# Kernel optimization log

Measured on AMD Instinct MI355X. Metric: run time of the kernel, lower is better.

## Reference

```python
import jax, jax.numpy as jnp
import numpy as np

EPS = 1e-5

def setup_inputs() -> dict:
    key = jax.random.key(0)
    ks = jax.random.split(key, 6)
    D, V, N = 2048, 30000, 4096
    return {
        "x": jax.random.normal(ks[0], (N, D), dtype=jnp.float32),
        "w1": jax.random.normal(ks[1], (D, D), dtype=jnp.float32) * (1.0 / np.sqrt(D)),
        "b1": jax.random.normal(ks[2], (D,), dtype=jnp.float32) * 0.02,
        "gamma": jnp.ones((D,), dtype=jnp.float32),
        "beta": jnp.zeros((D,), dtype=jnp.float32),
        "w3": jax.random.normal(ks[3], (V, D), dtype=jnp.float32) * (1.0 / np.sqrt(D)),
        "b3": jax.random.normal(ks[4], (V,), dtype=jnp.float32) * 0.02,
    }

def reference(x, w1, b1, gamma, beta, w3, b3):
    # Stage 1: Linear 2048 -> 2048 (torch convention: y = x @ W.T + b)
    h = jnp.einsum('nd,od->no', x, w1) + b1  # [N, 2048]
    # Stage 2: fused LayerNorm + Linear 2048 -> 30000
    mu = jnp.mean(h, axis=-1, keepdims=True)
    var = jnp.mean(jnp.square(h - mu), axis=-1, keepdims=True)
    hn = (h - mu) * jax.lax.rsqrt(var + EPS) * gamma + beta
    logits = jnp.einsum('nd,vd->nv', hn, w3) + b3  # [N, 30000]
    return logits
```

## Files before the change

### kernel.cpp

```cpp
#include <hip/hip_runtime.h>
#include <hip/hip_bf16.h>
#include <stdint.h>

typedef __attribute__((ext_vector_type(8))) short bf16x8;
typedef __attribute__((ext_vector_type(4))) float f32x4;

__device__ __forceinline__ uint16_t f2bf(float f) {
  uint32_t u = __builtin_bit_cast(uint32_t, f);
  u += 0x7fffu + ((u >> 16) & 1u);
  return (uint16_t)(u >> 16);
}

__global__ __launch_bounds__(256) void cvt_bf16(const float* __restrict__ in,
                                                uint16_t* __restrict__ out,
                                                size_t n8) {
  size_t i = (size_t)blockIdx.x * blockDim.x + threadIdx.x;
  size_t stride = (size_t)gridDim.x * blockDim.x;
  for (; i < n8; i += stride) {
    const float4* p = reinterpret_cast<const float4*>(in) + 2 * i;
    float4 a = p[0], b = p[1];
    uint4 o;
    o.x = (uint32_t)f2bf(a.x) | ((uint32_t)f2bf(a.y) << 16);
    o.y = (uint32_t)f2bf(a.z) | ((uint32_t)f2bf(a.w) << 16);
    o.z = (uint32_t)f2bf(b.x) | ((uint32_t)f2bf(b.y) << 16);
    o.w = (uint32_t)f2bf(b.z) | ((uint32_t)f2bf(b.w) << 16);
    reinterpret_cast<uint4*>(out)[i] = o;
  }
}

__global__ __launch_bounds__(256) void cvt_bf16_pad(const float* __restrict__ in,
                                                    uint16_t* __restrict__ out,
                                                    int rows_in, size_t n8) {
  size_t i = (size_t)blockIdx.x * blockDim.x + threadIdx.x;
  size_t stride = (size_t)gridDim.x * blockDim.x;
  for (; i < n8; i += stride) {
    size_t row = (i * 8) >> 11;
    uint4 o;
    if (row < (size_t)rows_in) {
      const float4* p = reinterpret_cast<const float4*>(in) + 2 * i;
      float4 a = p[0], b = p[1];
      o.x = (uint32_t)f2bf(a.x) | ((uint32_t)f2bf(a.y) << 16);
      o.y = (uint32_t)f2bf(a.z) | ((uint32_t)f2bf(a.w) << 16);
      o.z = (uint32_t)f2bf(b.x) | ((uint32_t)f2bf(b.y) << 16);
      o.w = (uint32_t)f2bf(b.z) | ((uint32_t)f2bf(b.w) << 16);
    } else {
      o.x = 0u; o.y = 0u; o.z = 0u; o.w = 0u;
    }
    reinterpret_cast<uint4*>(out)[i] = o;
  }
}

#define GLOAD16(g, l) __builtin_amdgcn_global_load_lds(                         \
    (__attribute__((address_space(1))) const void*)(g),                         \
    (__attribute__((address_space(3))) void*)(l), 16, 0, 0)

__global__ __launch_bounds__(256, 2) void gemm_bt_bf16(
    const uint16_t* __restrict__ A, const uint16_t* __restrict__ B,
    float* __restrict__ C, const float* __restrict__ bias,
    int M, int Npad, int K, int Nout)
{
  constexpr int BM = 128, BN = 128, BK = 32;
  __shared__ uint16_t sA[BM * BK];
  __shared__ uint16_t sB[BN * BK];

  const int ntile = Npad / BN;
  const int mtile = M / BM;
  const int nwg = ntile * mtile;
  const int bid = blockIdx.x;
  const int cpx = nwg >> 3;
  const int swz = (bid & 7) * cpx + (bid >> 3);
  const int tm = swz % mtile;
  const int tn = swz / mtile;

  const int tid = threadIdx.x;
  const int lane = tid & 63;
  const int wid = tid >> 6;
  const int wm = wid >> 1;
  const int wn = wid & 1;

  const int srow = tid >> 2;
  const int scol = (tid & 3) * 8;
  const uint16_t* ga0 = A + (size_t)(tm * BM + srow) * K + scol;
  const uint16_t* ga1 = ga0 + (size_t)64 * K;
  const uint16_t* gb0 = B + (size_t)(tn * BN + srow) * K + scol;
  const uint16_t* gb1 = gb0 + (size_t)64 * K;
  uint16_t* lA = sA + wid * 512;
  uint16_t* lB = sB + wid * 512;

  const int arow = wm * 64 + (lane & 15);
  const int brow = wn * 64 + (lane & 15);
  const int koff = (lane >> 4) * 8;

  f32x4 acc[4][4];
  #pragma unroll
  for (int m = 0; m < 4; ++m)
    #pragma unroll
    for (int n = 0; n < 4; ++n)
      acc[m][n] = (f32x4){0.f, 0.f, 0.f, 0.f};

  for (int k0 = 0; k0 < K; k0 += BK) {
    __syncthreads();
    GLOAD16(ga0, lA);
    GLOAD16(ga1, lA + 2048);
    GLOAD16(gb0, lB);
    GLOAD16(gb1, lB + 2048);
    ga0 += BK; ga1 += BK; gb0 += BK; gb1 += BK;
    __syncthreads();

    bf16x8 af[4], bfr[4];
    #pragma unroll
    for (int m = 0; m < 4; ++m)
      af[m] = *reinterpret_cast<const bf16x8*>(&sA[(arow + m * 16) * BK + koff]);
    #pragma unroll
    for (int n = 0; n < 4; ++n)
      bfr[n] = *reinterpret_cast<const bf16x8*>(&sB[(brow + n * 16) * BK + koff]);
    #pragma unroll
    for (int m = 0; m < 4; ++m)
      #pragma unroll
      for (int n = 0; n < 4; ++n)
        acc[m][n] = __builtin_amdgcn_mfma_f32_16x16x32_bf16(af[m], bfr[n],
                                                            acc[m][n], 0, 0, 0);
  }

  const int r0 = tm * BM + wm * 64 + (lane >> 4) * 4;
  const int c0 = tn * BN + wn * 64 + (lane & 15);
  #pragma unroll
  for (int m = 0; m < 4; ++m) {
    #pragma unroll
    for (int n = 0; n < 4; ++n) {
      const int c = c0 + n * 16;
      if (c < Nout) {
        const float bv = bias ? bias[c] : 0.f;
        #pragma unroll
        for (int j = 0; j < 4; ++j)
          C[(size_t)(r0 + m * 16 + j) * Nout + c] = acc[m][n][j] + bv;
      }
    }
  }
}

__global__ __launch_bounds__(256) void ln_bf16(
    const float* __restrict__ h, const float* __restrict__ b1,
    const float* __restrict__ gamma, const float* __restrict__ beta,
    uint16_t* __restrict__ out)
{
  constexpr int D = 2048;
  const int row = blockIdx.x;
  const int tid = threadIdx.x;
  const float* hp = h + (size_t)row * D + tid * 8;
  float v[8];
  {
    float4 a0 = *reinterpret_cast<const float4*>(hp);
    float4 a1 = *reinterpret_cast<const float4*>(hp + 4);
    float4 c0 = *reinterpret_cast<const float4*>(b1 + tid * 8);
    float4 c1 = *reinterpret_cast<const float4*>(b1 + tid * 8 + 4);
    v[0] = a0.x + c0.x; v[1] = a0.y + c0.y; v[2] = a0.z + c0.z; v[3] = a0.w + c0.w;
    v[4] = a1.x + c1.x; v[5] = a1.y + c1.y; v[6] = a1.z + c1.z; v[7] = a1.w + c1.w;
  }
  float s = 0.f, q = 0.f;
  #pragma unroll
  for (int i = 0; i < 8; ++i) { s += v[i]; q += v[i] * v[i]; }
  #pragma unroll
  for (int off = 32; off > 0; off >>= 1) {
    s += __shfl_down(s, off);
    q += __shfl_down(q, off);
  }
  __shared__ float red[8];
  const int wid = tid >> 6, lane = tid & 63;
  if (lane == 0) { red[wid] = s; red[4 + wid] = q; }
  __syncthreads();
  s = red[0] + red[1] + red[2] + red[3];
  q = red[4] + red[5] + red[6] + red[7];
  const float mu = s * (1.f / D);
  const float rs = rsqrtf(q * (1.f / D) - mu * mu + 1e-5f);
  float4 g0 = *reinterpret_cast<const float4*>(gamma + tid * 8);
  float4 g1 = *reinterpret_cast<const float4*>(gamma + tid * 8 + 4);
  float4 e0 = *reinterpret_cast<const float4*>(beta + tid * 8);
  float4 e1 = *reinterpret_cast<const float4*>(beta + tid * 8 + 4);
  const float g[8] = {g0.x, g0.y, g0.z, g0.w, g1.x, g1.y, g1.z, g1.w};
  const float e[8] = {e0.x, e0.y, e0.z, e0.w, e1.x, e1.y, e1.z, e1.w};
  uint32_t w[4];
  #pragma unroll
  for (int i = 0; i < 4; ++i) {
    float y0 = (v[2 * i]     - mu) * rs * g[2 * i]     + e[2 * i];
    float y1 = (v[2 * i + 1] - mu) * rs * g[2 * i + 1] + e[2 * i + 1];
    w[i] = (uint32_t)f2bf(y0) | ((uint32_t)f2bf(y1) << 16);
  }
  uint4 o; o.x = w[0]; o.y = w[1]; o.z = w[2]; o.w = w[3];
  reinterpret_cast<uint4*>(out + (size_t)row * D)[tid] = o;
}

extern "C" void kernel_launch(void* const* d_in, const int* in_sizes, int n_in,
                              void* d_out, int out_size, void* d_ws, size_t ws_size,
                              hipStream_t stream) {
  (void)in_sizes; (void)n_in; (void)out_size; (void)ws_size;
  const float* x     = (const float*)d_in[0];
  const float* w1    = (const float*)d_in[1];
  const float* b1    = (const float*)d_in[2];
  const float* gamma = (const float*)d_in[3];
  const float* beta  = (const float*)d_in[4];
  const float* w3    = (const float*)d_in[5];
  const float* b3    = (const float*)d_in[6];
  float* out = (float*)d_out;

  const int N = 4096, D = 2048, V = 30000, Vp = 30080;

  char* ws = (char*)d_ws;
  uint16_t* xb  = (uint16_t*)(ws);
  uint16_t* w1b = (uint16_t*)(ws + (16u  << 20));
  float*    h   = (float*)   (ws + (24u  << 20));
  uint16_t* hnb = (uint16_t*)(ws + (56u  << 20));
  uint16_t* w3b = (uint16_t*)(ws + (72u  << 20));

  hipLaunchKernelGGL(cvt_bf16, dim3(1024), dim3(256), 0, stream,
                     x, xb, (size_t)N * D / 8);
  hipLaunchKernelGGL(cvt_bf16, dim3(512), dim3(256), 0, stream,
                     w1, w1b, (size_t)D * D / 8);
  hipLaunchKernelGGL(cvt_bf16_pad, dim3(2048), dim3(256), 0, stream,
                     w3, w3b, V, (size_t)Vp * D / 8);
  hipLaunchKernelGGL(gemm_bt_bf16, dim3((N / 128) * (D / 128)), dim3(256), 0, stream,
                     xb, w1b, h, (const float*)nullptr, N, D, D, D);
  hipLaunchKernelGGL(ln_bf16, dim3(N), dim3(256), 0, stream,
                     h, b1, gamma, beta, hnb);
  hipLaunchKernelGGL(gemm_bt_bf16, dim3((N / 128) * (Vp / 128)), dim3(256), 0, stream,
                     hnb, w3b, out, b3, N, Vp, D, V);
}
```

Before: 1.371 ms.

## Add 256x256-tile multi-stage pipelined GEMM for vocab projection

Adds a 512-thread GEMM kernel with 256x256 output tiles and a four-buffer LDS ring (128KB) that keeps three global-to-LDS stages in flight, synchronised with explicit vmcnt waits and barriers. The large logits projection now uses this kernel, with the vocabulary padding raised to a multiple of 256. The goal is more operand reuse per LDS load and memory latency hidden behind MFMA work. The workspace is reshuffled and the w3 conversion moved after the layernorm so the bf16 weight buffer can reuse space no longer needed. The cost is higher register and LDS pressure, which limits the kernel to one workgroup per CU, plus slightly more wasted padding work.

```diff
diff --git a/kernel.cpp b/kernel.cpp
--- a/kernel.cpp
+++ b/kernel.cpp
@@ -139,6 +139,99 @@
   }
 }
 
+__global__ __launch_bounds__(512, 2) void gemm_bt_256(
+    const uint16_t* __restrict__ A, const uint16_t* __restrict__ B,
+    float* __restrict__ C, const float* __restrict__ bias,
+    int M, int Npad, int K, int Nout)
+{
+  __shared__ char lds[131072];
+  constexpr int BM = 256, BN = 256, BK = 32;
+  const int ntile = Npad / BN;
+  const int mtile = M / BM;
+  const int nwg = ntile * mtile;
+  const int bid = blockIdx.x;
+  const int cpx = nwg >> 3;
+  const int swz = (bid & 7) * cpx + (bid >> 3);
+  const int tm = swz % mtile;
+  const int tn = swz / mtile;
+
+  const int tid = threadIdx.x;
+  const int lane = tid & 63;
+  const int wid = tid >> 6;
+  const int wm = wid >> 2;
+  const int wn = wid & 3;
+
+  const size_t K_ = (size_t)K;
+  const uint16_t* gA = A + (size_t)(tm * BM + (tid >> 2)) * K_ + (tid & 3) * 8;
+  const uint16_t* gB = B + (size_t)(tn * BN + (tid >> 2)) * K_ + (tid & 3) * 8;
+  const size_t halfs = 128 * K_;
+  const int stageBase = wid * 1024;
+
+  const int nt = K / BK;
+
+  const int rd   = (lane & 15) * 64 + (lane >> 4) * 16;
+  const int aoff = wm * 8192 + rd;
+  const int boff = wn * 4096 + rd;
+
+  f32x4 acc[8][4];
+  #pragma unroll
+  for (int r = 0; r < 8; ++r)
+    #pragma unroll
+    for (int n = 0; n < 4; ++n)
+      acc[r][n] = (f32x4){0.f, 0.f, 0.f, 0.f};
+
+#define STAGE256(b, koff)                                                     \
+  { char* d = lds + (b) * 32768 + stageBase;                                  \
+    GLOAD16(gA + (koff),          d);                                         \
+    GLOAD16(gA + halfs + (koff),  d + 8192);                                  \
+    GLOAD16(gB + (koff),          d + 16384);                                 \
+    GLOAD16(gB + halfs + (koff),  d + 24576); }
+
+  STAGE256(0, 0); STAGE256(1, 32); STAGE256(2, 64);
+
+  for (int t = 0; t < nt; ++t) {
+    const int rem = nt - 1 - t;
+    if (rem >= 2)      asm volatile("s_waitcnt vmcnt(8)" ::: "memory");
+    else if (rem == 1) asm volatile("s_waitcnt vmcnt(4)" ::: "memory");
+    else               asm volatile("s_waitcnt vmcnt(0)" ::: "memory");
+    asm volatile("s_barrier" ::: "memory");
+    if (t + 3 < nt) STAGE256((t + 3) & 3, (t + 3) * BK);
+
+    const char* bA = lds + (t & 3) * 32768;
+    const char* bB = bA + 16384;
+    bf16x8 bF[4], aF[8];
+    #pragma unroll
+    for (int n = 0; n < 4; ++n)
+      bF[n] = *reinterpret_cast<const bf16x8*>(bB + boff + n * 1024);
+    #pragma unroll
+    for (int r = 0; r < 8; ++r)
+      aF[r] = *reinterpret_cast<const bf16x8*>(bA + aoff + r * 1024);
+    #pragma unroll
+    for (int r = 0; r < 8; ++r)
+      #pragma unroll
+      for (int n = 0; n < 4; ++n)
+        acc[r][n] = __builtin_amdgcn_mfma_f32_16x16x32_bf16(aF[r], bF[n],
+                                                            acc[r][n], 0, 0, 0);
+  }
+#undef STAGE256
+
+  const int r0 = tm * BM + wm * 128 + (lane >> 4) * 4;
+  const int c0 = tn * BN + wn * 64 + (lane & 15);
+  #pragma unroll
+  for (int r = 0; r < 8; ++r) {
+    #pragma unroll
+    for (int n = 0; n < 4; ++n) {
+      const int c = c0 + n * 16;
+      if (c < Nout) {
+        const float bv = bias ? bias[c] : 0.f;
+        #pragma unroll
+        for (int j = 0; j < 4; ++j)
+          C[(size_t)(r0 + r * 16 + j) * Nout + c] = acc[r][n][j] + bv;
+      }
+    }
+  }
+}
+
 __global__ __launch_bounds__(256) void ln_bf16(
     const float* __restrict__ h, const float* __restrict__ b1,
     const float* __restrict__ gamma, const float* __restrict__ beta,
@@ -203,25 +296,25 @@
   const float* b3    = (const float*)d_in[6];
   float* out = (float*)d_out;
 
-  const int N = 4096, D = 2048, V = 30000, Vp = 30080;
+  const int N = 4096, D = 2048, V = 30000, Vp = 30208;
 
   char* ws = (char*)d_ws;
-  uint16_t* xb  = (uint16_t*)(ws);
-  uint16_t* w1b = (uint16_t*)(ws + (16u  << 20));
-  float*    h   = (float*)   (ws + (24u  << 20));
-  uint16_t* hnb = (uint16_t*)(ws + (56u  << 20));
-  uint16_t* w3b = (uint16_t*)(ws + (72u  << 20));
+  uint16_t* hnb = (uint16_t*)(ws);
+  float*    h   = (float*)   (ws + (16u << 20));
+  uint16_t* xb  = (uint16_t*)(ws + (48u << 20));
+  uint16_t* w1b = (uint16_t*)(ws + (64u << 20));
+  uint16_t* w3b = (uint16_t*)(ws + (24u << 20));
 
   hipLaunchKernelGGL(cvt_bf16, dim3(1024), dim3(256), 0, stream,
                      x, xb, (size_t)N * D / 8);
   hipLaunchKernelGGL(cvt_bf16, dim3(512), dim3(256), 0, stream,
                      w1, w1b, (size_t)D * D / 8);
-  hipLaunchKernelGGL(cvt_bf16_pad, dim3(2048), dim3(256), 0, stream,
-                     w3, w3b, V, (size_t)Vp * D / 8);
   hipLaunchKernelGGL(gemm_bt_bf16, dim3((N / 128) * (D / 128)), dim3(256), 0, stream,
                      xb, w1b, h, (const float*)nullptr, N, D, D, D);
   hipLaunchKernelGGL(ln_bf16, dim3(N), dim3(256), 0, stream,
                      h, b1, gamma, beta, hnb);
-  hipLaunchKernelGGL(gemm_bt_bf16, dim3((N / 128) * (Vp / 128)), dim3(256), 0, stream,
+  hipLaunchKernelGGL(cvt_bf16_pad, dim3(2048), dim3(256), 0, stream,
+                     w3, w3b, V, (size_t)Vp * D / 8);
+  hipLaunchKernelGGL(gemm_bt_256, dim3((N / 256) * (Vp / 256)), dim3(512), 0, stream,
                      hnb, w3b, out, b3, N, Vp, D, V);
 }
```

Measured after the change: 1.264 ms. 1.08x faster.
